# Performance work log

Measured on AMD Instinct MI355X. Metric: run time of the kernel, lower is better.

The kernel has to match this reference:

```python
import jax, jax.numpy as jnp
import numpy as np

COST_CLASS = 1.0
COST_BBOX = 1.0
COST_GIOU = 1.0
COST_MASK_CE = 1.0
COST_MASK_DICE = 1.0
ALPHA = 0.25   # hardcoded in forward (focal alpha)
GAMMA = 2.0


def box_cxcywh_to_xyxy(b):
    cx, cy, w, h = jnp.split(b, 4, axis=-1)
    return jnp.concatenate([cx - 0.5 * w, cy - 0.5 * h, cx + 0.5 * w, cy + 0.5 * h], axis=-1)


def generalized_box_iou(b1, b2):
    # b1 [N,4], b2 [M,4] in xyxy -> [N,M]
    a1 = (b1[:, 2] - b1[:, 0]) * (b1[:, 3] - b1[:, 1])
    a2 = (b2[:, 2] - b2[:, 0]) * (b2[:, 3] - b2[:, 1])
    lt = jnp.maximum(b1[:, None, :2], b2[None, :, :2])
    rb = jnp.minimum(b1[:, None, 2:], b2[None, :, 2:])
    wh = jnp.clip(rb - lt, 0.0)
    inter = wh[..., 0] * wh[..., 1]
    union = a1[:, None] + a2[None, :] - inter
    iou = inter / union
    ltc = jnp.minimum(b1[:, None, :2], b2[None, :, :2])
    rbc = jnp.maximum(b1[:, None, 2:], b2[None, :, 2:])
    whc = jnp.clip(rbc - ltc, 0.0)
    area = whc[..., 0] * whc[..., 1]
    return iou - (area - union) / area


def point_sample_bilinear(masks, coords):
    # masks [N,H,W], coords [P,2] in [0,1] (x,y); grid_sample align_corners=False,
    # zero padding: pixel = coord*size - 0.5. Fully batched over N and P.
    H, W = masks.shape[-2:]
    x = coords[:, 0] * W - 0.5
    y = coords[:, 1] * H - 0.5
    x0 = jnp.floor(x); y0 = jnp.floor(y)
    wx = x - x0; wy = y - y0
    x0i = x0.astype(jnp.int32); y0i = y0.astype(jnp.int32)
    def g(yi, xi):
        valid = ((xi >= 0) & (xi < W) & (yi >= 0) & (yi < H)).astype(masks.dtype)
        v = masks[:, jnp.clip(yi, 0, H - 1), jnp.clip(xi, 0, W - 1)]  # [N,P]
        return v * valid
    return (g(y0i, x0i) * (1 - wy) * (1 - wx) + g(y0i, x0i + 1) * (1 - wy) * wx
            + g(y0i + 1, x0i) * wy * (1 - wx) + g(y0i + 1, x0i + 1) * wy * wx)


def point_sample_nearest(masks, coords):
    H, W = masks.shape[-2:]
    xi = jnp.round(coords[:, 0] * W - 0.5).astype(jnp.int32)
    yi = jnp.round(coords[:, 1] * H - 0.5).astype(jnp.int32)
    valid = ((xi >= 0) & (xi < W) & (yi >= 0) & (yi < H)).astype(masks.dtype)
    return masks[:, jnp.clip(yi, 0, H - 1), jnp.clip(xi, 0, W - 1)] * valid


def _cost_single(logits, boxes, labels, tboxes, pmasks, tmasks, pts):
    # logits [Q,C], boxes [Q,4], labels [T], tboxes [T,4],
    # pmasks [Q,H,W], tmasks [T,H,W] (0/1 int), pts [P,2]
    prob = jax.nn.sigmoid(logits)
    neg_cost = (1 - ALPHA) * prob ** GAMMA * (-jax.nn.log_sigmoid(-logits))
    pos_cost = ALPHA * (1 - prob) ** GAMMA * (-jax.nn.log_sigmoid(logits))
    cost_class = jnp.take(pos_cost, labels, axis=1) - jnp.take(neg_cost, labels, axis=1)  # [Q,T]
    giou = generalized_box_iou(box_cxcywh_to_xyxy(boxes), box_cxcywh_to_xyxy(tboxes))
    cost_bbox = jnp.abs(boxes[:, None, :] - tboxes[None, :, :]).sum(-1)  # L1 cdist
    C = COST_BBOX * cost_bbox + COST_CLASS * cost_class - COST_GIOU * giou
    # batched point sampling (replaces per-query / per-target python loops)
    pm = point_sample_bilinear(pmasks, pts)                    # [Q,P]
    tm = point_sample_nearest(tmasks.astype(pmasks.dtype), pts)  # [T,P]
    P = pm.shape[-1]
    # batch_sigmoid_ce_loss: pairwise BCE-with-logits, mean over points
    pos_ce = jax.nn.softplus(-pm)  # loss if target==1
    neg_ce = jax.nn.softplus(pm)   # loss if target==0
    ce = (pos_ce @ tm.T + neg_ce @ (1.0 - tm).T) / P
    # batch_dice_loss
    sm = jax.nn.sigmoid(pm)
    num = 2.0 * (sm @ tm.T)
    den = sm.sum(-1)[:, None] + tm.sum(-1)[None, :]
    dice = 1.0 - (num + 1.0) / (den + 1.0)
    C = C + COST_MASK_CE * ce + COST_MASK_DICE * dice
    # replicate C[C.isinf()|C.isnan()] = 2*max
    finite = jnp.isfinite(C)
    mx = jnp.max(jnp.where(finite, C, -jnp.inf))
    return jnp.where(finite, C, 2.0 * mx)


def setup_inputs() -> dict:
    key = jax.random.key(0)
    ks = jax.random.split(key, 7)
    bs, Q, C, T, H, W = 2, 900, 91, 100, 128, 128
    P = H * W // 16  # mask_point_sample_ratio = 16
    return {
        "pred_logits": jax.random.normal(ks[0], (bs, Q, C), jnp.float32),
        "pred_boxes": jax.random.uniform(ks[1], (bs, Q, 4), jnp.float32),
        "tgt_labels": jax.random.randint(ks[2], (bs, T), 0, C, jnp.int32),
        "tgt_boxes": jax.random.uniform(ks[3], (bs, T, 4), jnp.float32),
        "pred_masks": jax.random.normal(ks[4], (bs, Q, H, W), jnp.float32),
        "tgt_masks": jax.random.randint(ks[5], (bs, T, H, W), 0, 2, jnp.int32),
        "point_coords": jax.random.uniform(ks[6], (bs, P, 2), jnp.float32),
    }


def reference(pred_logits, pred_boxes, tgt_labels, tgt_boxes, pred_masks, tgt_masks, point_coords):
    # Returns the per-image matching cost matrices [bs, Q, T]; the CPU-side
    # Hungarian solve (scipy linear_sum_assignment) consumes these.
    return jax.vmap(_cost_single)(pred_logits, pred_boxes, tgt_labels, tgt_boxes,
                                  pred_masks, tgt_masks, point_coords)
```

## Files before the change

kernel.cpp:

```cpp
#include <hip/hip_runtime.h>
#include <math.h>

#define QN 900
#define TN 100
#define CN 91
#define PN 1024
#define HWD 128
#define BS 2

__device__ __forceinline__ float sigmoidf_(float x) {
    return 1.0f / (1.0f + __expf(-x));
}
__device__ __forceinline__ float softplusf_(float x) {
    return fmaxf(x, 0.0f) + __logf(1.0f + __expf(-fabsf(x)));
}
__device__ __forceinline__ unsigned bfhi(float f) {
    unsigned u = __float_as_uint(f);
    return (u + 0x7FFFu + ((u >> 16) & 1u)) & 0xFFFF0000u;
}

__global__ __launch_bounds__(256) void prep_kernel(
    const float2* __restrict__ coords, const int* __restrict__ tmasks,
    unsigned* __restrict__ tmw, float* __restrict__ tmsum)
{
    __shared__ int cnt[4];
    const int bx = blockIdx.x;
    const int tid = threadIdx.x;
    const int wv = tid >> 6, lane = tid & 63;
    const int b = bx / TN, t = bx % TN;
    const int* m = tmasks + (size_t)(b * TN + t) * (HWD * HWD);
    int addr[4]; unsigned vld[4];
#pragma unroll
    for (int c = 0; c < 4; ++c) {
        float2 cd = coords[b * PN + c * 256 + tid];
        int xi = (int)rintf(cd.x * (float)HWD - 0.5f);
        int yi = (int)rintf(cd.y * (float)HWD - 0.5f);
        vld[c] = (xi >= 0) & (xi < HWD) & (yi >= 0) & (yi < HWD);
        addr[c] = min(max(yi, 0), HWD - 1) * HWD + min(max(xi, 0), HWD - 1);
    }
    int rv[4];
#pragma unroll
    for (int c = 0; c < 4; ++c) rv[c] = m[addr[c]];
    int mycnt = 0;
#pragma unroll
    for (int c = 0; c < 4; ++c) {
        unsigned long long bal = __ballot(vld[c] && (rv[c] != 0));
        if (lane == 0) {
            tmw[(size_t)(b * TN + t) * 32 + c * 8 + wv * 2 + 0] = (unsigned)(bal & 0xFFFFFFFFull);
            tmw[(size_t)(b * TN + t) * 32 + c * 8 + wv * 2 + 1] = (unsigned)(bal >> 32);
            mycnt += __popcll(bal);
        }
    }
    if (lane == 0) cnt[wv] = mycnt;
    __syncthreads();
    if (tid == 0)
        tmsum[b * TN + t] = (float)((cnt[0] + cnt[1]) + (cnt[2] + cnt[3]));
}

__global__ __launch_bounds__(256, 4) void main_kernel(
    const float* __restrict__ logits, const float4* __restrict__ pboxes,
    const int* __restrict__ labels, const float4* __restrict__ tboxes,
    const float* __restrict__ pmasks, const float2* __restrict__ coords,
    const unsigned* __restrict__ tmw, const float* __restrict__ tmsum_,
    float* __restrict__ out, float* __restrict__ blockmax,
    int* __restrict__ badflag)
{
    __shared__ unsigned pl[PN];
    __shared__ float part[8][32][9];
    __shared__ float sred[8];
    __shared__ float mred[256];
    __shared__ int sbad;

    const int bq = blockIdx.x;
    const int b = bq / QN, q = bq - b * QN;
    const int tid = threadIdx.x;
    const int wv = tid >> 6, lane = tid & 63;
    const int pc = tid >> 5, ts = tid & 31;
    const float* mask = pmasks + (size_t)bq * (HWD * HWD);

    if (tid == 0) sbad = 0;

    int a00[4], a01[4], a10[4], a11[4];
    float wxa[4], wya[4];
    unsigned fl[4];
#pragma unroll
    for (int c = 0; c < 4; ++c) {
        float2 cd = coords[b * PN + c * 256 + tid];
        float x = cd.x * (float)HWD - 0.5f;
        float y = cd.y * (float)HWD - 0.5f;
        float fx = floorf(x), fy = floorf(y);
        int x0 = (int)fx, y0 = (int)fy;
        int x1 = x0 + 1, y1 = y0 + 1;
        wxa[c] = x - fx; wya[c] = y - fy;
        int xc0 = min(max(x0, 0), HWD - 1), xc1 = min(max(x1, 0), HWD - 1);
        int yc0 = min(max(y0, 0), HWD - 1), yc1 = min(max(y1, 0), HWD - 1);
        a00[c] = yc0 * HWD + xc0; a01[c] = yc0 * HWD + xc1;
        a10[c] = yc1 * HWD + xc0; a11[c] = yc1 * HWD + xc1;
        fl[c] = (unsigned)((x0 >= 0) & (x0 < HWD))
              | ((unsigned)((x1 >= 0) & (x1 < HWD)) << 1)
              | ((unsigned)((y0 >= 0) & (y0 < HWD)) << 2)
              | ((unsigned)((y1 >= 0) & (y1 < HWD)) << 3);
    }

    float r00[4], r01[4], r10[4], r11[4];
#pragma unroll
    for (int c = 0; c < 4; ++c) {
        r00[c] = mask[a00[c]];
        r01[c] = mask[a01[c]];
        r10[c] = mask[a10[c]];
        r11[c] = mask[a11[c]];
    }

    const unsigned* rowb = tmw + (size_t)b * TN * 32;
    unsigned w0[4], w1[4], w2[4], w3[4];
#pragma unroll
    for (int g = 0; g < 4; ++g) {
        w0[g] = rowb[(ts +  0) * 32 + pc * 4 + g];
        w1[g] = rowb[(ts + 32) * 32 + pc * 4 + g];
        w2[g] = rowb[(ts + 64) * 32 + pc * 4 + g];
        w3[g] = (ts + 96 < TN) ? rowb[(ts + 96) * 32 + pc * 4 + g] : 0u;
    }
    float lg = 0.f, tsum = 0.f;
    float4 tb = make_float4(0, 0, 0, 0), pb = make_float4(0, 0, 0, 0);
    if (tid < TN) {
        int lab = labels[b * TN + tid];
        lg = logits[(size_t)(b * QN + q) * CN + lab];
        tsum = tmsum_[b * TN + tid];
        tb = tboxes[b * TN + tid];
        pb = pboxes[b * QN + q];
    }

    float lsp = 0.f, lsm = 0.f;
#pragma unroll
    for (int c = 0; c < 4; ++c) {
        bool bx0 = fl[c] & 1u, bx1 = fl[c] & 2u, by0 = fl[c] & 4u, by1 = fl[c] & 8u;
        float v00 = (by0 && bx0) ? r00[c] : 0.f;
        float v01 = (by0 && bx1) ? r01[c] : 0.f;
        float v10 = (by1 && bx0) ? r10[c] : 0.f;
        float v11 = (by1 && bx1) ? r11[c] : 0.f;
        float wx = wxa[c], wy = wya[c];
        float pm = (v00 * (1.f - wx) + v01 * wx) * (1.f - wy) +
                   (v10 * (1.f - wx) + v11 * wx) * wy;
        float sg = sigmoidf_(pm);
        lsp += softplusf_(pm);
        lsm += sg;
        pl[c * 256 + tid] = bfhi(pm) | (bfhi(sg) >> 16);
    }
    for (int off = 32; off > 0; off >>= 1) {
        lsp += __shfl_down(lsp, off);
        lsm += __shfl_down(lsm, off);
    }
    if (lane == 0) { sred[wv * 2 + 0] = lsp; sred[wv * 2 + 1] = lsm; }
    __syncthreads();
    float s_sp = (sred[0] + sred[2]) + (sred[4] + sred[6]);
    float s_sm = (sred[1] + sred[3]) + (sred[5] + sred[7]);

    float a0 = 0, a1 = 0, a2 = 0, a3 = 0, a4 = 0, a5 = 0, a6 = 0, a7 = 0;
    {
        const uint4* plv = (const uint4*)&pl[pc * 128];
        uint4 ua = plv[0];
        uint4 ub = plv[1];
#pragma unroll
        for (int it = 0; it < 32; ++it) {
            const int g = it >> 3, sh = (it & 7) * 4;
            uint4 ucur = ua;
            ua = ub;
            if (it < 30) ub = plv[it + 2];
            unsigned q0 = w0[g] >> sh;
            unsigned q1 = w1[g] >> sh;
            unsigned q2 = w2[g] >> sh;
            unsigned q3 = w3[g] >> sh;
#pragma unroll
            for (int k = 0; k < 4; ++k) {
                unsigned uv = (k == 0) ? ucur.x : (k == 1) ? ucur.y : (k == 2) ? ucur.z : ucur.w;
                float pmv = __uint_as_float(uv & 0xFFFF0000u);
                float sgv = __uint_as_float(uv << 16);
                float f0 = (float)((q0 >> k) & 1u);
                float f1 = (float)((q1 >> k) & 1u);
                float f2 = (float)((q2 >> k) & 1u);
                float f3 = (float)((q3 >> k) & 1u);
                a0 = fmaf(pmv, f0, a0); a1 = fmaf(sgv, f0, a1);
                a2 = fmaf(pmv, f1, a2); a3 = fmaf(sgv, f1, a3);
                a4 = fmaf(pmv, f2, a4); a5 = fmaf(sgv, f2, a5);
                a6 = fmaf(pmv, f3, a6); a7 = fmaf(sgv, f3, a7);
            }
        }
    }
    part[pc][ts][0] = a0; part[pc][ts][1] = a1;
    part[pc][ts][2] = a2; part[pc][ts][3] = a3;
    part[pc][ts][4] = a4; part[pc][ts][5] = a5;
    part[pc][ts][6] = a6; part[pc][ts][7] = a7;
    __syncthreads();

    float val = -INFINITY;
    if (tid < TN) {
        int t = tid, tss = t & 31, kk = t >> 5;
        float apm = 0.f, asg = 0.f;
#pragma unroll
        for (int pp = 0; pp < 8; ++pp) {
            apm += part[pp][tss][kk * 2 + 0];
            asg += part[pp][tss][kk * 2 + 1];
        }
        float ce = (s_sp - apm) * (1.0f / (float)PN);
        float dice = 1.0f - (2.0f * asg + 1.0f) / (s_sm + tsum + 1.0f);

        float pr = sigmoidf_(lg);
        float cls = 0.25f * (1.f - pr) * (1.f - pr) * softplusf_(-lg)
                  - 0.75f * pr * pr * softplusf_(lg);

        float l1 = fabsf(pb.x - tb.x) + fabsf(pb.y - tb.y) +
                   fabsf(pb.z - tb.z) + fabsf(pb.w - tb.w);

        float px1 = pb.x - 0.5f * pb.z, py1 = pb.y - 0.5f * pb.w;
        float px2 = pb.x + 0.5f * pb.z, py2 = pb.y + 0.5f * pb.w;
        float tx1 = tb.x - 0.5f * tb.z, ty1 = tb.y - 0.5f * tb.w;
        float tx2 = tb.x + 0.5f * tb.z, ty2 = tb.y + 0.5f * tb.w;
        float A1 = (px2 - px1) * (py2 - py1);
        float A2 = (tx2 - tx1) * (ty2 - ty1);
        float iw = fmaxf(fminf(px2, tx2) - fmaxf(px1, tx1), 0.f);
        float ih = fmaxf(fminf(py2, ty2) - fmaxf(py1, ty1), 0.f);
        float inter = iw * ih;
        float uni = A1 + A2 - inter;
        float iou = inter / uni;
        float cw = fmaxf(fmaxf(px2, tx2) - fminf(px1, tx1), 0.f);
        float chh = fmaxf(fmaxf(py2, ty2) - fminf(py1, ty1), 0.f);
        float area = cw * chh;
        float giou = iou - (area - uni) / area;

        float Cv = l1 + cls - giou + ce + dice;
        out[(size_t)(b * QN + q) * TN + t] = Cv;
        if (isfinite(Cv)) val = Cv;
        else sbad = 1;
    }
    mred[tid] = val;
    __syncthreads();
    if (tid < 64) {
        float m = fmaxf(fmaxf(mred[tid], mred[tid + 64]),
                        fmaxf(mred[tid + 128], mred[tid + 192]));
        for (int off = 32; off > 0; off >>= 1)
            m = fmaxf(m, __shfl_down(m, off));
        if (tid == 0) { blockmax[bq] = m; badflag[bq] = sbad; }
    }
}

__global__ __launch_bounds__(128) void fix_kernel(float* __restrict__ out,
                                                  const float* __restrict__ blockmax,
                                                  const int* __restrict__ badflag)
{
    const int bq = blockIdx.x;
    if (badflag[bq] == 0) return;
    const int tid = threadIdx.x;
    if (tid >= TN) return;
    const int b = bq / QN;
    float v = out[(size_t)bq * TN + tid];
    if (!isfinite(v)) {
        float m = -INFINITY;
        for (int k = 0; k < QN; ++k) m = fmaxf(m, blockmax[b * QN + k]);
        out[(size_t)bq * TN + tid] = 2.0f * m;
    }
}

extern "C" void kernel_launch(void* const* d_in, const int* in_sizes, int n_in,
                              void* d_out, int out_size, void* d_ws, size_t ws_size,
                              hipStream_t stream) {
    const float* logits  = (const float*)d_in[0];
    const float4* pboxes = (const float4*)d_in[1];
    const int* labels    = (const int*)d_in[2];
    const float4* tboxes = (const float4*)d_in[3];
    const float* pmasks  = (const float*)d_in[4];
    const int* tmasks    = (const int*)d_in[5];
    const float* coords  = (const float*)d_in[6];
    float* out = (float*)d_out;

    char* ws = (char*)d_ws;
    unsigned* tmw   = (unsigned*)(ws);
    float* tmsum    = (float*)(ws + 25600);
    float* blockmax = (float*)(ws + 26400);
    int* badflag    = (int*)(ws + 33600);

    hipLaunchKernelGGL(prep_kernel, dim3(BS * TN), dim3(256), 0, stream,
                       (const float2*)coords, tmasks, tmw, tmsum);
    hipLaunchKernelGGL(main_kernel, dim3(BS * QN), dim3(256), 0, stream,
                       logits, pboxes, labels, tboxes, pmasks, (const float2*)coords,
                       tmw, tmsum, out, blockmax, badflag);
    hipLaunchKernelGGL(fix_kernel, dim3(BS * QN), dim3(128), 0, stream,
                       out, blockmax, badflag);
}
```

Baseline: 54.95 us.

## Split sampling into bf16 planes and compute mask costs with MFMA GEMM

```diff
diff --git a/kernel.cpp b/kernel.cpp
--- a/kernel.cpp
+++ b/kernel.cpp
@@ -7,6 +7,11 @@
 #define PN 1024
 #define HWD 128
 #define BS 2
+#define QT 57
+#define TPAD 112
+
+typedef __bf16 bf16x8 __attribute__((ext_vector_type(8)));
+typedef float f32x4 __attribute__((ext_vector_type(4)));
 
 __device__ __forceinline__ float sigmoidf_(float x) {
     return 1.0f / (1.0f + __expf(-x));
@@ -14,249 +19,243 @@
 __device__ __forceinline__ float softplusf_(float x) {
     return fmaxf(x, 0.0f) + __logf(1.0f + __expf(-fabsf(x)));
 }
-__device__ __forceinline__ unsigned bfhi(float f) {
+__device__ __forceinline__ unsigned short bfrne(float f) {
     unsigned u = __float_as_uint(f);
-    return (u + 0x7FFFu + ((u >> 16) & 1u)) & 0xFFFF0000u;
-}
-
-__global__ __launch_bounds__(256) void prep_kernel(
+    return (unsigned short)((u + 0x7FFFu + ((u >> 16) & 1u)) >> 16);
+}
+
+__global__ __launch_bounds__(256) void stage1_kernel(
     const float2* __restrict__ coords, const int* __restrict__ tmasks,
-    unsigned* __restrict__ tmw, float* __restrict__ tmsum)
+    const float* __restrict__ pmasks, unsigned short* __restrict__ plane_pm,
+    unsigned short* __restrict__ plane_sg, unsigned short* __restrict__ tmbT,
+    float* __restrict__ tmsum, float2* __restrict__ ssum)
 {
+    __shared__ float sred[8];
     __shared__ int cnt[4];
     const int bx = blockIdx.x;
     const int tid = threadIdx.x;
     const int wv = tid >> 6, lane = tid & 63;
-    const int b = bx / TN, t = bx % TN;
-    const int* m = tmasks + (size_t)(b * TN + t) * (HWD * HWD);
-    int addr[4]; unsigned vld[4];
-#pragma unroll
-    for (int c = 0; c < 4; ++c) {
-        float2 cd = coords[b * PN + c * 256 + tid];
-        int xi = (int)rintf(cd.x * (float)HWD - 0.5f);
-        int yi = (int)rintf(cd.y * (float)HWD - 0.5f);
-        vld[c] = (xi >= 0) & (xi < HWD) & (yi >= 0) & (yi < HWD);
-        addr[c] = min(max(yi, 0), HWD - 1) * HWD + min(max(xi, 0), HWD - 1);
-    }
-    int rv[4];
-#pragma unroll
-    for (int c = 0; c < 4; ++c) rv[c] = m[addr[c]];
-    int mycnt = 0;
-#pragma unroll
-    for (int c = 0; c < 4; ++c) {
-        unsigned long long bal = __ballot(vld[c] && (rv[c] != 0));
-        if (lane == 0) {
-            tmw[(size_t)(b * TN + t) * 32 + c * 8 + wv * 2 + 0] = (unsigned)(bal & 0xFFFFFFFFull);
-            tmw[(size_t)(b * TN + t) * 32 + c * 8 + wv * 2 + 1] = (unsigned)(bal >> 32);
-            mycnt += __popcll(bal);
-        }
-    }
-    if (lane == 0) cnt[wv] = mycnt;
-    __syncthreads();
-    if (tid == 0)
-        tmsum[b * TN + t] = (float)((cnt[0] + cnt[1]) + (cnt[2] + cnt[3]));
-}
-
-__global__ __launch_bounds__(256, 4) void main_kernel(
+
+    if (bx < BS * QN) {
+        const int b = bx / QN;
+        const float* mask = pmasks + (size_t)bx * (HWD * HWD);
+
+        int a00[4], a01[4], a10[4], a11[4];
+        float wxa[4], wya[4];
+        unsigned fl[4];
+#pragma unroll
+        for (int c = 0; c < 4; ++c) {
+            float2 cd = coords[b * PN + c * 256 + tid];
+            float x = cd.x * (float)HWD - 0.5f;
+            float y = cd.y * (float)HWD - 0.5f;
+            float fx = floorf(x), fy = floorf(y);
+            int x0 = (int)fx, y0 = (int)fy;
+            int x1 = x0 + 1, y1 = y0 + 1;
+            wxa[c] = x - fx; wya[c] = y - fy;
+            int xc0 = min(max(x0, 0), HWD - 1), xc1 = min(max(x1, 0), HWD - 1);
+            int yc0 = min(max(y0, 0), HWD - 1), yc1 = min(max(y1, 0), HWD - 1);
+            a00[c] = yc0 * HWD + xc0; a01[c] = yc0 * HWD + xc1;
+            a10[c] = yc1 * HWD + xc0; a11[c] = yc1 * HWD + xc1;
+            fl[c] = (unsigned)((x0 >= 0) & (x0 < HWD))
+                  | ((unsigned)((x1 >= 0) & (x1 < HWD)) << 1)
+                  | ((unsigned)((y0 >= 0) & (y0 < HWD)) << 2)
+                  | ((unsigned)((y1 >= 0) & (y1 < HWD)) << 3);
+        }
+        float r00[4], r01[4], r10[4], r11[4];
+#pragma unroll
+        for (int c = 0; c < 4; ++c) {
+            r00[c] = mask[a00[c]];
+            r01[c] = mask[a01[c]];
+            r10[c] = mask[a10[c]];
+            r11[c] = mask[a11[c]];
+        }
+        float lsp = 0.f, lsm = 0.f;
+#pragma unroll
+        for (int c = 0; c < 4; ++c) {
+            bool bx0 = fl[c] & 1u, bx1 = fl[c] & 2u, by0 = fl[c] & 4u, by1 = fl[c] & 8u;
+            float v00 = (by0 && bx0) ? r00[c] : 0.f;
+            float v01 = (by0 && bx1) ? r01[c] : 0.f;
+            float v10 = (by1 && bx0) ? r10[c] : 0.f;
+            float v11 = (by1 && bx1) ? r11[c] : 0.f;
+            float wx = wxa[c], wy = wya[c];
+            float pm = (v00 * (1.f - wx) + v01 * wx) * (1.f - wy) +
+                       (v10 * (1.f - wx) + v11 * wx) * wy;
+            float sg = sigmoidf_(pm);
+            lsp += softplusf_(pm);
+            lsm += sg;
+            const size_t po = (size_t)(b * (QT * 16) + (bx - b * QN)) * PN + c * 256 + tid;
+            plane_pm[po] = bfrne(pm);
+            plane_sg[po] = bfrne(sg);
+        }
+        for (int off = 32; off > 0; off >>= 1) {
+            lsp += __shfl_down(lsp, off);
+            lsm += __shfl_down(lsm, off);
+        }
+        if (lane == 0) { sred[wv * 2 + 0] = lsp; sred[wv * 2 + 1] = lsm; }
+        __syncthreads();
+        if (tid == 0)
+            ssum[bx] = make_float2((sred[0] + sred[2]) + (sred[4] + sred[6]),
+                                   (sred[1] + sred[3]) + (sred[5] + sred[7]));
+    } else {
+        const int bt = bx - BS * QN;
+        const int b = bt / TN, t = bt % TN;
+        const int* m = tmasks + (size_t)(b * TN + t) * (HWD * HWD);
+        int addr[4]; unsigned vld[4];
+#pragma unroll
+        for (int c = 0; c < 4; ++c) {
+            float2 cd = coords[b * PN + c * 256 + tid];
+            int xi = (int)rintf(cd.x * (float)HWD - 0.5f);
+            int yi = (int)rintf(cd.y * (float)HWD - 0.5f);
+            vld[c] = (xi >= 0) & (xi < HWD) & (yi >= 0) & (yi < HWD);
+            addr[c] = min(max(yi, 0), HWD - 1) * HWD + min(max(xi, 0), HWD - 1);
+        }
+        int rv[4];
+#pragma unroll
+        for (int c = 0; c < 4; ++c) rv[c] = m[addr[c]];
+        int mycnt = 0;
+#pragma unroll
+        for (int c = 0; c < 4; ++c) {
+            const int bit = (vld[c] && (rv[c] != 0)) ? 1 : 0;
+            tmbT[(size_t)(b * TPAD + t) * PN + c * 256 + tid] =
+                bit ? (unsigned short)0x3F80 : (unsigned short)0;
+            unsigned long long bal = __ballot(bit);
+            if (lane == 0) mycnt += __popcll(bal);
+        }
+        if (lane == 0) cnt[wv] = mycnt;
+        __syncthreads();
+        if (tid == 0)
+            tmsum[b * TN + t] = (float)((cnt[0] + cnt[1]) + (cnt[2] + cnt[3]));
+    }
+}
+
+__global__ __launch_bounds__(256) void gemm_kernel(
     const float* __restrict__ logits, const float4* __restrict__ pboxes,
     const int* __restrict__ labels, const float4* __restrict__ tboxes,
-    const float* __restrict__ pmasks, const float2* __restrict__ coords,
-    const unsigned* __restrict__ tmw, const float* __restrict__ tmsum_,
+    const unsigned short* __restrict__ plane_pm,
+    const unsigned short* __restrict__ plane_sg,
+    const unsigned short* __restrict__ tmbT,
+    const float* __restrict__ tmsum_, const float2* __restrict__ ssum,
     float* __restrict__ out, float* __restrict__ blockmax,
     int* __restrict__ badflag)
 {
-    __shared__ unsigned pl[PN];
-    __shared__ float part[8][32][9];
-    __shared__ float sred[8];
-    __shared__ float mred[256];
-    __shared__ int sbad;
-
-    const int bq = blockIdx.x;
-    const int b = bq / QN, q = bq - b * QN;
+    __shared__ float wmax_s[4];
+    __shared__ int wbad_s[4];
+
+    const int bid = blockIdx.x;
+    const int b = bid / QT, tile = bid - b * QT;
+    const int q0 = tile * 16;
     const int tid = threadIdx.x;
-    const int wv = tid >> 6, lane = tid & 63;
-    const int pc = tid >> 5, ts = tid & 31;
-    const float* mask = pmasks + (size_t)bq * (HWD * HWD);
-
-    if (tid == 0) sbad = 0;
-
-    int a00[4], a01[4], a10[4], a11[4];
-    float wxa[4], wya[4];
-    unsigned fl[4];
-#pragma unroll
-    for (int c = 0; c < 4; ++c) {
-        float2 cd = coords[b * PN + c * 256 + tid];
-        float x = cd.x * (float)HWD - 0.5f;
-        float y = cd.y * (float)HWD - 0.5f;
-        float fx = floorf(x), fy = floorf(y);
-        int x0 = (int)fx, y0 = (int)fy;
-        int x1 = x0 + 1, y1 = y0 + 1;
-        wxa[c] = x - fx; wya[c] = y - fy;
-        int xc0 = min(max(x0, 0), HWD - 1), xc1 = min(max(x1, 0), HWD - 1);
-        int yc0 = min(max(y0, 0), HWD - 1), yc1 = min(max(y1, 0), HWD - 1);
-        a00[c] = yc0 * HWD + xc0; a01[c] = yc0 * HWD + xc1;
-        a10[c] = yc1 * HWD + xc0; a11[c] = yc1 * HWD + xc1;
-        fl[c] = (unsigned)((x0 >= 0) & (x0 < HWD))
-              | ((unsigned)((x1 >= 0) & (x1 < HWD)) << 1)
-              | ((unsigned)((y0 >= 0) & (y0 < HWD)) << 2)
-              | ((unsigned)((y1 >= 0) & (y1 < HWD)) << 3);
-    }
-
-    float r00[4], r01[4], r10[4], r11[4];
-#pragma unroll
-    for (int c = 0; c < 4; ++c) {
-        r00[c] = mask[a00[c]];
-        r01[c] = mask[a01[c]];
-        r10[c] = mask[a10[c]];
-        r11[c] = mask[a11[c]];
-    }
-
-    const unsigned* rowb = tmw + (size_t)b * TN * 32;
-    unsigned w0[4], w1[4], w2[4], w3[4];
-#pragma unroll
-    for (int g = 0; g < 4; ++g) {
-        w0[g] = rowb[(ts +  0) * 32 + pc * 4 + g];
-        w1[g] = rowb[(ts + 32) * 32 + pc * 4 + g];
-        w2[g] = rowb[(ts + 64) * 32 + pc * 4 + g];
-        w3[g] = (ts + 96 < TN) ? rowb[(ts + 96) * 32 + pc * 4 + g] : 0u;
-    }
-    float lg = 0.f, tsum = 0.f;
-    float4 tb = make_float4(0, 0, 0, 0), pb = make_float4(0, 0, 0, 0);
-    if (tid < TN) {
-        int lab = labels[b * TN + tid];
-        lg = logits[(size_t)(b * QN + q) * CN + lab];
-        tsum = tmsum_[b * TN + tid];
-        tb = tboxes[b * TN + tid];
-        pb = pboxes[b * QN + q];
-    }
-
-    float lsp = 0.f, lsm = 0.f;
-#pragma unroll
-    for (int c = 0; c < 4; ++c) {
-        bool bx0 = fl[c] & 1u, bx1 = fl[c] & 2u, by0 = fl[c] & 4u, by1 = fl[c] & 8u;
-        float v00 = (by0 && bx0) ? r00[c] : 0.f;
-        float v01 = (by0 && bx1) ? r01[c] : 0.f;
-        float v10 = (by1 && bx0) ? r10[c] : 0.f;
-        float v11 = (by1 && bx1) ? r11[c] : 0.f;
-        float wx = wxa[c], wy = wya[c];
-        float pm = (v00 * (1.f - wx) + v01 * wx) * (1.f - wy) +
-                   (v10 * (1.f - wx) + v11 * wx) * wy;
-        float sg = sigmoidf_(pm);
-        lsp += softplusf_(pm);
-        lsm += sg;
-        pl[c * 256 + tid] = bfhi(pm) | (bfhi(sg) >> 16);
-    }
-    for (int off = 32; off > 0; off >>= 1) {
-        lsp += __shfl_down(lsp, off);
-        lsm += __shfl_down(lsm, off);
-    }
-    if (lane == 0) { sred[wv * 2 + 0] = lsp; sred[wv * 2 + 1] = lsm; }
+    const int w = tid >> 6, lane = tid & 63;
+    const int lr = lane & 15;
+    const int lk = (lane >> 4) * 8;
+    const int n0 = w;
+    const int n1 = w + 4;
+    const bool has1 = (n1 < 7);
+
+    const size_t arow = (size_t)(b * (QT * 16) + q0 + lr) * PN + lk;
+    const size_t brow0 = (size_t)(b * TPAD + n0 * 16 + lr) * PN + lk;
+    const size_t brow1 = (size_t)(b * TPAD + (has1 ? n1 : n0) * 16 + lr) * PN + lk;
+
+    f32x4 aP0 = {0.f, 0.f, 0.f, 0.f}, aS0 = {0.f, 0.f, 0.f, 0.f};
+    f32x4 aP1 = {0.f, 0.f, 0.f, 0.f}, aS1 = {0.f, 0.f, 0.f, 0.f};
+#pragma unroll 4
+    for (int ks = 0; ks < 32; ++ks) {
+        const int ko = ks * 32;
+        bf16x8 af = *(const bf16x8*)(plane_pm + arow + ko);
+        bf16x8 ag = *(const bf16x8*)(plane_sg + arow + ko);
+        bf16x8 b0 = *(const bf16x8*)(tmbT + brow0 + ko);
+        bf16x8 b1 = *(const bf16x8*)(tmbT + brow1 + ko);
+        aP0 = __builtin_amdgcn_mfma_f32_16x16x32_bf16(af, b0, aP0, 0, 0, 0);
+        aS0 = __builtin_amdgcn_mfma_f32_16x16x32_bf16(ag, b0, aS0, 0, 0, 0);
+        aP1 = __builtin_amdgcn_mfma_f32_16x16x32_bf16(af, b1, aP1, 0, 0, 0);
+        aS1 = __builtin_amdgcn_mfma_f32_16x16x32_bf16(ag, b1, aS1, 0, 0, 0);
+    }
+
+    float wmaxv = -INFINITY;
+    int wbad = 0;
+#pragma unroll
+    for (int which = 0; which < 2; ++which) {
+        if (which && !has1) break;
+        const int n = which ? n1 : n0;
+        const int t = n * 16 + lr;
+        const bool tok = (t < TN);
+        float tsum = 0.f; float4 tb = make_float4(0, 0, 0, 0); int lab = 0;
+        if (tok) {
+            tsum = tmsum_[b * TN + t];
+            tb = tboxes[b * TN + t];
+            lab = labels[b * TN + t];
+        }
+        const f32x4 ap = which ? aP1 : aP0;
+        const f32x4 as = which ? aS1 : aS0;
+#pragma unroll
+        for (int r = 0; r < 4; ++r) {
+            const int q = q0 + (lane >> 4) * 4 + r;
+            if (!tok || q >= QN) continue;
+            float2 ss = ssum[b * QN + q];
+            float lg = logits[(size_t)(b * QN + q) * CN + lab];
+            float4 pb = pboxes[b * QN + q];
+            float apm = ap[r], asg = as[r];
+
+            float ce = (ss.x - apm) * (1.0f / (float)PN);
+            float dice = 1.0f - (2.0f * asg + 1.0f) / (ss.y + tsum + 1.0f);
+
+            float pr = sigmoidf_(lg);
+            float cls = 0.25f * (1.f - pr) * (1.f - pr) * softplusf_(-lg)
+                      - 0.75f * pr * pr * softplusf_(lg);
+
+            float l1 = fabsf(pb.x - tb.x) + fabsf(pb.y - tb.y) +
+                       fabsf(pb.z - tb.z) + fabsf(pb.w - tb.w);
+
+            float px1 = pb.x - 0.5f * pb.z, py1 = pb.y - 0.5f * pb.w;
+            float px2 = pb.x + 0.5f * pb.z, py2 = pb.y + 0.5f * pb.w;
+            float tx1 = tb.x - 0.5f * tb.z, ty1 = tb.y - 0.5f * tb.w;
+            float tx2 = tb.x + 0.5f * tb.z, ty2 = tb.y + 0.5f * tb.w;
+            float A1 = (px2 - px1) * (py2 - py1);
+            float A2 = (tx2 - tx1) * (ty2 - ty1);
+            float iw = fmaxf(fminf(px2, tx2) - fmaxf(px1, tx1), 0.f);
+            float ih = fmaxf(fminf(py2, ty2) - fmaxf(py1, ty1), 0.f);
+            float inter = iw * ih;
+            float uni = A1 + A2 - inter;
+            float iou = inter / uni;
+            float cw = fmaxf(fmaxf(px2, tx2) - fminf(px1, tx1), 0.f);
+            float chh = fmaxf(fmaxf(py2, ty2) - fminf(py1, ty1), 0.f);
+            float area = cw * chh;
+            float giou = iou - (area - uni) / area;
+
+            float Cv = l1 + cls - giou + ce + dice;
+            out[(size_t)(b * QN + q) * TN + t] = Cv;
+            if (isfinite(Cv)) wmaxv = fmaxf(wmaxv, Cv);
+            else wbad = 1;
+        }
+    }
+    for (int off = 32; off > 0; off >>= 1)
+        wmaxv = fmaxf(wmaxv, __shfl_down(wmaxv, off));
+    wbad = (__ballot(wbad) != 0ull) ? 1 : 0;
+    if (lane == 0) { wmax_s[w] = wmaxv; wbad_s[w] = wbad; }
     __syncthreads();
-    float s_sp = (sred[0] + sred[2]) + (sred[4] + sred[6]);
-    float s_sm = (sred[1] + sred[3]) + (sred[5] + sred[7]);
-
-    float a0 = 0, a1 = 0, a2 = 0, a3 = 0, a4 = 0, a5 = 0, a6 = 0, a7 = 0;
-    {
-        const uint4* plv = (const uint4*)&pl[pc * 128];
-        uint4 ua = plv[0];
-        uint4 ub = plv[1];
-#pragma unroll
-        for (int it = 0; it < 32; ++it) {
-            const int g = it >> 3, sh = (it & 7) * 4;
-            uint4 ucur = ua;
-            ua = ub;
-            if (it < 30) ub = plv[it + 2];
-            unsigned q0 = w0[g] >> sh;
-            unsigned q1 = w1[g] >> sh;
-            unsigned q2 = w2[g] >> sh;
-            unsigned q3 = w3[g] >> sh;
-#pragma unroll
-            for (int k = 0; k < 4; ++k) {
-                unsigned uv = (k == 0) ? ucur.x : (k == 1) ? ucur.y : (k == 2) ? ucur.z : ucur.w;
-                float pmv = __uint_as_float(uv & 0xFFFF0000u);
-                float sgv = __uint_as_float(uv << 16);
-                float f0 = (float)((q0 >> k) & 1u);
-                float f1 = (float)((q1 >> k) & 1u);
-                float f2 = (float)((q2 >> k) & 1u);
-                float f3 = (float)((q3 >> k) & 1u);
-                a0 = fmaf(pmv, f0, a0); a1 = fmaf(sgv, f0, a1);
-                a2 = fmaf(pmv, f1, a2); a3 = fmaf(sgv, f1, a3);
-                a4 = fmaf(pmv, f2, a4); a5 = fmaf(sgv, f2, a5);
-                a6 = fmaf(pmv, f3, a6); a7 = fmaf(sgv, f3, a7);
-            }
-        }
-    }
-    part[pc][ts][0] = a0; part[pc][ts][1] = a1;
-    part[pc][ts][2] = a2; part[pc][ts][3] = a3;
-    part[pc][ts][4] = a4; part[pc][ts][5] = a5;
-    part[pc][ts][6] = a6; part[pc][ts][7] = a7;
-    __syncthreads();
-
-    float val = -INFINITY;
-    if (tid < TN) {
-        int t = tid, tss = t & 31, kk = t >> 5;
-        float apm = 0.f, asg = 0.f;
-#pragma unroll
-        for (int pp = 0; pp < 8; ++pp) {
-            apm += part[pp][tss][kk * 2 + 0];
-            asg += part[pp][tss][kk * 2 + 1];
-        }
-        float ce = (s_sp - apm) * (1.0f / (float)PN);
-        float dice = 1.0f - (2.0f * asg + 1.0f) / (s_sm + tsum + 1.0f);
-
-        float pr = sigmoidf_(lg);
-        float cls = 0.25f * (1.f - pr) * (1.f - pr) * softplusf_(-lg)
-                  - 0.75f * pr * pr * softplusf_(lg);
-
-        float l1 = fabsf(pb.x - tb.x) + fabsf(pb.y - tb.y) +
-                   fabsf(pb.z - tb.z) + fabsf(pb.w - tb.w);
-
-        float px1 = pb.x - 0.5f * pb.z, py1 = pb.y - 0.5f * pb.w;
-        float px2 = pb.x + 0.5f * pb.z, py2 = pb.y + 0.5f * pb.w;
-        float tx1 = tb.x - 0.5f * tb.z, ty1 = tb.y - 0.5f * tb.w;
-        float tx2 = tb.x + 0.5f * tb.z, ty2 = tb.y + 0.5f * tb.w;
-        float A1 = (px2 - px1) * (py2 - py1);
-        float A2 = (tx2 - tx1) * (ty2 - ty1);
-        float iw = fmaxf(fminf(px2, tx2) - fmaxf(px1, tx1), 0.f);
-        float ih = fmaxf(fminf(py2, ty2) - fmaxf(py1, ty1), 0.f);
-        float inter = iw * ih;
-        float uni = A1 + A2 - inter;
-        float iou = inter / uni;
-        float cw = fmaxf(fmaxf(px2, tx2) - fminf(px1, tx1), 0.f);
-        float chh = fmaxf(fmaxf(py2, ty2) - fminf(py1, ty1), 0.f);
-        float area = cw * chh;
-        float giou = iou - (area - uni) / area;
-
-        float Cv = l1 + cls - giou + ce + dice;
-        out[(size_t)(b * QN + q) * TN + t] = Cv;
-        if (isfinite(Cv)) val = Cv;
-        else sbad = 1;
-    }
-    mred[tid] = val;
-    __syncthreads();
-    if (tid < 64) {
-        float m = fmaxf(fmaxf(mred[tid], mred[tid + 64]),
-                        fmaxf(mred[tid + 128], mred[tid + 192]));
-        for (int off = 32; off > 0; off >>= 1)
-            m = fmaxf(m, __shfl_down(m, off));
-        if (tid == 0) { blockmax[bq] = m; badflag[bq] = sbad; }
-    }
-}
-
-__global__ __launch_bounds__(128) void fix_kernel(float* __restrict__ out,
+    if (tid == 0) {
+        float m = fmaxf(fmaxf(wmax_s[0], wmax_s[1]), fmaxf(wmax_s[2], wmax_s[3]));
+        blockmax[bid] = m;
+        badflag[bid] = wbad_s[0] | wbad_s[1] | wbad_s[2] | wbad_s[3];
+    }
+}
+
+__global__ __launch_bounds__(256) void fix_kernel(float* __restrict__ out,
                                                   const float* __restrict__ blockmax,
                                                   const int* __restrict__ badflag)
 {
-    const int bq = blockIdx.x;
-    if (badflag[bq] == 0) return;
-    const int tid = threadIdx.x;
-    if (tid >= TN) return;
-    const int b = bq / QN;
-    float v = out[(size_t)bq * TN + tid];
-    if (!isfinite(v)) {
-        float m = -INFINITY;
-        for (int k = 0; k < QN; ++k) m = fmaxf(m, blockmax[b * QN + k]);
-        out[(size_t)bq * TN + tid] = 2.0f * m;
+    const int bid = blockIdx.x;
+    if (badflag[bid] == 0) return;
+    const int b = bid / QT, tile = bid - b * QT;
+    const int q0 = tile * 16;
+    float m = -INFINITY;
+    for (int k = 0; k < QT; ++k) m = fmaxf(m, blockmax[b * QT + k]);
+    for (int idx = threadIdx.x; idx < 16 * TN; idx += 256) {
+        const int q = q0 + idx / TN;
+        if (q >= QN) break;
+        const size_t o = (size_t)(b * QN + q) * TN + (idx % TN);
+        float v = out[o];
+        if (!isfinite(v)) out[o] = 2.0f * m;
     }
 }
 
@@ -273,16 +272,20 @@
     float* out = (float*)d_out;
 
     char* ws = (char*)d_ws;
-    unsigned* tmw   = (unsigned*)(ws);
-    float* tmsum    = (float*)(ws + 25600);
-    float* blockmax = (float*)(ws + 26400);
-    int* badflag    = (int*)(ws + 33600);
-
-    hipLaunchKernelGGL(prep_kernel, dim3(BS * TN), dim3(256), 0, stream,
-                       (const float2*)coords, tmasks, tmw, tmsum);
-    hipLaunchKernelGGL(main_kernel, dim3(BS * QN), dim3(256), 0, stream,
-                       logits, pboxes, labels, tboxes, pmasks, (const float2*)coords,
-                       tmw, tmsum, out, blockmax, badflag);
-    hipLaunchKernelGGL(fix_kernel, dim3(BS * QN), dim3(128), 0, stream,
+    unsigned short* plane_pm = (unsigned short*)(ws);
+    unsigned short* plane_sg = (unsigned short*)(ws + 3735552);
+    unsigned short* tmbT     = (unsigned short*)(ws + 7471104);
+    float* tmsum    = (float*)(ws + 7929856);
+    float2* ssum    = (float2*)(ws + 7930656);
+    float* blockmax = (float*)(ws + 7945056);
+    int* badflag    = (int*)(ws + 7945520);
+
+    hipLaunchKernelGGL(stage1_kernel, dim3(BS * QN + BS * TN), dim3(256), 0, stream,
+                       (const float2*)coords, tmasks, pmasks, plane_pm, plane_sg,
+                       tmbT, tmsum, ssum);
+    hipLaunchKernelGGL(gemm_kernel, dim3(BS * QT), dim3(256), 0, stream,
+                       logits, pboxes, labels, tboxes, plane_pm, plane_sg, tmbT,
+                       tmsum, ssum, out, blockmax, badflag);
+    hipLaunchKernelGGL(fix_kernel, dim3(BS * QT), dim3(256), 0, stream,
                        out, blockmax, badflag);
 }
```

After: 56.05 us. +2.0%, slower.
